# Performance work log

Measured on AMD Instinct MI355X. Metric: run time of the kernel, lower is better.

## Reference

```python
import jax, jax.numpy as jnp
import numpy as np

PATCH_SIZE = 16
PATCH_STRIDE = 8
LEVEL = 3

# pywt db4 decomposition filters (dec_lo, dec_hi)
_DB4_DEC_LO = np.array([-0.010597401784997278, 0.032883011666982945,
                        0.030841381835986965, -0.18703481171888114,
                        -0.02798376941698385, 0.6308807679295904,
                        0.7148465705525415, 0.23037781330885523], dtype=np.float32)
_DB4_DEC_HI = np.array([-0.23037781330885523, 0.7148465705525415,
                        -0.6308807679295904, -0.02798376941698385,
                        0.18703481171888114, 0.030841381835986965,
                        -0.032883011666982945, -0.010597401784997278], dtype=np.float32)


def _swt(x, level):
    """Undecimated (a-trous) SWT with periodic boundary, ptwt convention.
    x: (BN, T) with T divisible by 2**level. Returns [cA_L, cD_L, ..., cD_1]."""
    # torch conv1d is cross-correlation -> use flipped filters (true convolution)
    filt = jnp.stack([jnp.asarray(_DB4_DEC_LO[::-1].copy()),
                      jnp.asarray(_DB4_DEC_HI[::-1].copy())], axis=0)[:, None, :]  # (2,1,8)
    filt = filt.astype(x.dtype)
    flen = filt.shape[-1]
    res_lo = x[:, None, :]  # (BN, 1, T)
    details = []
    for lvl in range(level):
        d = 2 ** lvl
        padl, padr = d * (flen // 2 - 1), d * (flen // 2)
        xp = jnp.concatenate([res_lo[..., -padl:], res_lo, res_lo[..., :padr]], axis=-1)
        res = jax.lax.conv_general_dilated(
            xp, filt, window_strides=(1,), padding='VALID',
            rhs_dilation=(d,), dimension_numbers=('NCH', 'OIH', 'NCH'))  # (BN,2,T)
        res_lo = res[:, :1, :]
        details.append(res[:, 1, :])
    return [res_lo[:, 0, :]] + details[::-1]


def setup_inputs() -> dict:
    key = jax.random.key(0)
    x = jax.random.normal(key, (64, 4096, 32), dtype=jnp.float32)
    return {"x": x}


def reference(x):
    B, T, N = x.shape
    xt = jnp.transpose(x, (0, 2, 1))  # (B, N, T)
    pow2 = 2 ** LEVEL
    pad_len = (-T) % pow2
    if pad_len:
        xt = jnp.pad(xt, ((0, 0), (0, 0), (0, pad_len)), mode='edge')  # replicate
    T_pad = T + pad_len
    coeffs = _swt(xt.reshape(B * N, T_pad), LEVEL)           # (level+1) x (BN, T_pad)
    cs = jnp.stack(coeffs, axis=1).reshape(B, N, LEVEL + 1, T_pad)
    if pad_len:
        cs = cs[..., :T]
    P = (T - PATCH_SIZE) // PATCH_STRIDE + 1
    idx = jnp.arange(P)[:, None] * PATCH_STRIDE + jnp.arange(PATCH_SIZE)[None, :]
    patches = cs[..., idx]                                   # (B, N, L+1, P, p)
    patches = jnp.transpose(patches, (0, 3, 1, 2, 4))        # (B, P, N, L+1, p)
    return patches.reshape(B * P, N * (LEVEL + 1), PATCH_SIZE)
```

## Files before the change

kernel.cpp:

```cpp
#include <hip/hip_runtime.h>


#define T_LEN    4096
#define T_MASK   4095
#define NPATCH   511
#define NCHAN    32
#define NTHREADS 256

__device__ __constant__ float c_lo[8] = {
    -0.010597401784997278f, 0.032883011666982945f, 0.030841381835986965f,
    -0.18703481171888114f, -0.02798376941698385f, 0.6308807679295904f,
    0.7148465705525415f,   0.23037781330885523f};
__device__ __constant__ float c_hi[8] = {
    -0.23037781330885523f, 0.7148465705525415f, -0.6308807679295904f,
    -0.02798376941698385f, 0.18703481171888114f, 0.030841381835986965f,
    -0.032883011666982945f, -0.010597401784997278f};

__device__ __forceinline__ void store_pair(float* __restrict__ out_bn, int cbase,
                                           const float* __restrict__ bufLo,
                                           const float* __restrict__ bufHi, int tid) {
#pragma unroll
    for (int it = 0; it < 16; ++it) {
        const int e4 = tid + it * NTHREADS;
        if (e4 < NPATCH * 8) {
            const int p    = e4 >> 3;
            const int r    = e4 & 7;
            const int csub = r >> 2;
            const int j0   = (r & 3) * 4;
            const float* src = csub ? bufHi : bufLo;
            const float4 v = *(const float4*)&src[8 * p + j0];
            *(float4*)&out_bn[(size_t)p * 2048 + (cbase + csub) * 16 + j0] = v;
        }
    }
}

__global__ __launch_bounds__(NTHREADS, 2) void swt_patch(const float* __restrict__ x,
                                                         float* __restrict__ out) {
    __shared__ float bufX[T_LEN];
    __shared__ float bufA[T_LEN];
    __shared__ float bufDa[T_LEN];
    __shared__ float bufDb[T_LEN];

    const int i = blockIdx.x;
    const int r = i & 7;
    const int q = i >> 3;
    const int b = r + 8 * (q >> 5);
    const int n = q & 31;
    const int tid = threadIdx.x;

    const float* xp = x + (size_t)b * T_LEN * NCHAN + n;
#pragma unroll
    for (int k = 0; k < 16; ++k) {
        const int t = tid + k * NTHREADS;
        bufX[t] = xp[(size_t)t * NCHAN];
    }
    __syncthreads();

    float* out_bn = out + (size_t)b * NPATCH * 2048 + (size_t)n * 64;
    const float4* X4 = (const float4*)bufX;
    const float4* A4 = (const float4*)bufA;

#pragma unroll
    for (int k = 0; k < 4; ++k) {
        const int t4 = 4 * (tid + k * NTHREADS);
        float w[12];
        *(float4*)&w[0] = X4[((t4 - 4) & T_MASK) >> 2];
        *(float4*)&w[4] = X4[t4 >> 2];
        *(float4*)&w[8] = X4[((t4 + 4) & T_MASK) >> 2];
        float4 va, vd;
        float* pa = (float*)&va; float* pd = (float*)&vd;
#pragma unroll
        for (int ii = 0; ii < 4; ++ii) {
            float sa = 0.f, sd = 0.f;
#pragma unroll
            for (int j = 0; j < 8; ++j) {
                const float v = w[ii + 8 - j];
                sa = fmaf(c_lo[j], v, sa);
                sd = fmaf(c_hi[j], v, sd);
            }
            pa[ii] = sa; pd[ii] = sd;
        }
        ((float4*)bufA)[t4 >> 2]  = va;
        ((float4*)bufDa)[t4 >> 2] = vd;
    }
    __syncthreads();

#pragma unroll
    for (int k = 0; k < 4; ++k) {
        const int t4 = 4 * (tid + k * NTHREADS);
        float w[20];
        *(float4*)&w[0]  = A4[((t4 - 8) & T_MASK) >> 2];
        *(float4*)&w[4]  = A4[((t4 - 4) & T_MASK) >> 2];
        *(float4*)&w[8]  = A4[t4 >> 2];
        *(float4*)&w[12] = A4[((t4 + 4) & T_MASK) >> 2];
        *(float4*)&w[16] = A4[((t4 + 8) & T_MASK) >> 2];
        float4 va, vd;
        float* pa = (float*)&va; float* pd = (float*)&vd;
#pragma unroll
        for (int ii = 0; ii < 4; ++ii) {
            float sa = 0.f, sd = 0.f;
#pragma unroll
            for (int j = 0; j < 8; ++j) {
                const float v = w[ii + 16 - 2 * j];
                sa = fmaf(c_lo[j], v, sa);
                sd = fmaf(c_hi[j], v, sd);
            }
            pa[ii] = sa; pd[ii] = sd;
        }
        ((float4*)bufX)[t4 >> 2]  = va;
        ((float4*)bufDb)[t4 >> 2] = vd;
    }
    __syncthreads();

    store_pair(out_bn, 2, bufDb, bufDa, tid);
    __syncthreads();

#pragma unroll
    for (int k = 0; k < 4; ++k) {
        const int t4 = 4 * (tid + k * NTHREADS);
        float w[32];
#pragma unroll
        for (int c4 = 0; c4 < 8; ++c4)
            *(float4*)&w[4 * c4] = X4[((t4 - 12 + 4 * c4) & T_MASK) >> 2];
        float4 va, vd;
        float* pa = (float*)&va; float* pd = (float*)&vd;
#pragma unroll
        for (int ii = 0; ii < 4; ++ii) {
            float sa = 0.f, sd = 0.f;
#pragma unroll
            for (int j = 0; j < 8; ++j) {
                const float v = w[ii + 28 - 4 * j];
                sa = fmaf(c_lo[j], v, sa);
                sd = fmaf(c_hi[j], v, sd);
            }
            pa[ii] = sa; pd[ii] = sd;
        }
        ((float4*)bufA)[t4 >> 2]  = va;
        ((float4*)bufDa)[t4 >> 2] = vd;
    }
    __syncthreads();

    store_pair(out_bn, 0, bufA, bufDa, tid);
}

extern "C" void kernel_launch(void* const* d_in, const int* in_sizes, int n_in,
                              void* d_out, int out_size, void* d_ws, size_t ws_size,
                              hipStream_t stream) {
    const float* x = (const float*)d_in[0];
    float* out = (float*)d_out;
    hipLaunchKernelGGL(swt_patch, dim3(64 * 32), dim3(NTHREADS), 0, stream, x, out);
}
```

Baseline: 318.3 us.

## Tile SWT over time chunks with halo, covering all channels per block

Each block now handles one 64-sample time chunk for all 32 channels of a batch, loading a haloed window with coalesced float4 reads and transposing it into padded shared memory. The three SWT levels are computed on shrinking halo ranges. Results are staged so each block writes a contiguous span of output patches with fully coalesced float4 stores. This replaces the old strided per-channel loads and scattered 64-byte output writes, at the cost of recomputing halo samples and using more, smaller blocks.

```diff
diff --git a/kernel.cpp b/kernel.cpp
--- a/kernel.cpp
+++ b/kernel.cpp
@@ -1,11 +1,19 @@
 #include <hip/hip_runtime.h>
 
 
-#define T_LEN    4096
+#define NTHREADS 256
 #define T_MASK   4095
-#define NPATCH   511
-#define NCHAN    32
-#define NTHREADS 256
+
+#define S_IN  132
+#define S_A1  116
+#define S_A2  108
+#define S_ST  76
+#define OFF_IN 0
+#define OFF_A1 4224
+#define OFF_A2 0
+#define OFF_ST 7936
+#define ST_C   2436
+#define LDS_FLOATS (OFF_ST + 4*ST_C)
 
 __device__ __constant__ float c_lo[8] = {
     -0.010597401784997278f, 0.032883011666982945f, 0.030841381835986965f,
@@ -16,57 +24,42 @@
     -0.02798376941698385f, 0.18703481171888114f, 0.030841381835986965f,
     -0.032883011666982945f, -0.010597401784997278f};
 
-__device__ __forceinline__ void store_pair(float* __restrict__ out_bn, int cbase,
-                                           const float* __restrict__ bufLo,
-                                           const float* __restrict__ bufHi, int tid) {
-#pragma unroll
-    for (int it = 0; it < 16; ++it) {
-        const int e4 = tid + it * NTHREADS;
-        if (e4 < NPATCH * 8) {
-            const int p    = e4 >> 3;
-            const int r    = e4 & 7;
-            const int csub = r >> 2;
-            const int j0   = (r & 3) * 4;
-            const float* src = csub ? bufHi : bufLo;
-            const float4 v = *(const float4*)&src[8 * p + j0];
-            *(float4*)&out_bn[(size_t)p * 2048 + (cbase + csub) * 16 + j0] = v;
-        }
-    }
-}
-
 __global__ __launch_bounds__(NTHREADS, 2) void swt_patch(const float* __restrict__ x,
                                                          float* __restrict__ out) {
-    __shared__ float bufX[T_LEN];
-    __shared__ float bufA[T_LEN];
-    __shared__ float bufDa[T_LEN];
-    __shared__ float bufDb[T_LEN];
+    __shared__ float lds[LDS_FLOATS];
 
-    const int i = blockIdx.x;
-    const int r = i & 7;
-    const int q = i >> 3;
-    const int b = r + 8 * (q >> 5);
-    const int n = q & 31;
+    const int blk = blockIdx.x;
+    const int b   = blk >> 6;
+    const int cid = blk & 63;
+    const int T0  = cid << 6;
+    const int p0  = cid << 3;
     const int tid = threadIdx.x;
 
-    const float* xp = x + (size_t)b * T_LEN * NCHAN + n;
+    const float* xb = x + (size_t)b * (4096 * 32);
+    {
 #pragma unroll
-    for (int k = 0; k < 16; ++k) {
-        const int t = tid + k * NTHREADS;
-        bufX[t] = xp[(size_t)t * NCHAN];
+        for (int it = 0; it < 4; ++it) {
+            const int id = tid + it * NTHREADS;
+            const int i  = id >> 3;
+            const int n0 = (id & 7) * 4;
+            const int t  = (T0 - 23 + i) & T_MASK;
+            const float4 v = *(const float4*)&xb[(size_t)t * 32 + n0];
+            lds[OFF_IN + (n0 + 0) * S_IN + i] = v.x;
+            lds[OFF_IN + (n0 + 1) * S_IN + i] = v.y;
+            lds[OFF_IN + (n0 + 2) * S_IN + i] = v.z;
+            lds[OFF_IN + (n0 + 3) * S_IN + i] = v.w;
+        }
     }
     __syncthreads();
 
-    float* out_bn = out + (size_t)b * NPATCH * 2048 + (size_t)n * 64;
-    const float4* X4 = (const float4*)bufX;
-    const float4* A4 = (const float4*)bufA;
-
-#pragma unroll
-    for (int k = 0; k < 4; ++k) {
-        const int t4 = 4 * (tid + k * NTHREADS);
+    for (int tsk = tid; tsk < 29 * 32; tsk += NTHREADS) {
+        const int n = tsk & 31, q = tsk >> 5;
+        const int trel0 = -20 + 4 * q;
         float w[12];
-        *(float4*)&w[0] = X4[((t4 - 4) & T_MASK) >> 2];
-        *(float4*)&w[4] = X4[t4 >> 2];
-        *(float4*)&w[8] = X4[((t4 + 4) & T_MASK) >> 2];
+        const int base = OFF_IN + n * S_IN + 4 * q;
+        *(float4*)&w[0] = *(const float4*)&lds[base];
+        *(float4*)&w[4] = *(const float4*)&lds[base + 4];
+        *(float4*)&w[8] = *(const float4*)&lds[base + 8];
         float4 va, vd;
         float* pa = (float*)&va; float* pd = (float*)&vd;
 #pragma unroll
@@ -74,26 +67,26 @@
             float sa = 0.f, sd = 0.f;
 #pragma unroll
             for (int j = 0; j < 8; ++j) {
-                const float v = w[ii + 8 - j];
+                const float v = w[ii + 7 - j];
                 sa = fmaf(c_lo[j], v, sa);
                 sd = fmaf(c_hi[j], v, sd);
             }
             pa[ii] = sa; pd[ii] = sd;
         }
-        ((float4*)bufA)[t4 >> 2]  = va;
-        ((float4*)bufDa)[t4 >> 2] = vd;
+        *(float4*)&lds[OFF_A1 + n * S_A1 + (trel0 + 20)] = va;
+        if (trel0 >= 0 && trel0 <= 68)
+            *(float4*)&lds[OFF_ST + 3 * ST_C + n * S_ST + trel0] = vd;
     }
     __syncthreads();
 
+    for (int tsk = tid; tsk < 25 * 32; tsk += NTHREADS) {
+        const int n = tsk & 31, q = tsk >> 5;
+        const int trel0 = -12 + 4 * q;
+        float w[20];
+        const int base = OFF_A1 + n * S_A1 + 4 * q;
 #pragma unroll
-    for (int k = 0; k < 4; ++k) {
-        const int t4 = 4 * (tid + k * NTHREADS);
-        float w[20];
-        *(float4*)&w[0]  = A4[((t4 - 8) & T_MASK) >> 2];
-        *(float4*)&w[4]  = A4[((t4 - 4) & T_MASK) >> 2];
-        *(float4*)&w[8]  = A4[t4 >> 2];
-        *(float4*)&w[12] = A4[((t4 + 4) & T_MASK) >> 2];
-        *(float4*)&w[16] = A4[((t4 + 8) & T_MASK) >> 2];
+        for (int c4 = 0; c4 < 5; ++c4)
+            *(float4*)&w[4 * c4] = *(const float4*)&lds[base + 4 * c4];
         float4 va, vd;
         float* pa = (float*)&va; float* pd = (float*)&vd;
 #pragma unroll
@@ -107,21 +100,20 @@
             }
             pa[ii] = sa; pd[ii] = sd;
         }
-        ((float4*)bufX)[t4 >> 2]  = va;
-        ((float4*)bufDb)[t4 >> 2] = vd;
+        *(float4*)&lds[OFF_A2 + n * S_A2 + (trel0 + 12)] = va;
+        if (trel0 >= 0 && trel0 <= 68)
+            *(float4*)&lds[OFF_ST + 2 * ST_C + n * S_ST + trel0] = vd;
     }
     __syncthreads();
 
-    store_pair(out_bn, 2, bufDb, bufDa, tid);
-    __syncthreads();
-
-#pragma unroll
-    for (int k = 0; k < 4; ++k) {
-        const int t4 = 4 * (tid + k * NTHREADS);
+    for (int tsk = tid; tsk < 18 * 32; tsk += NTHREADS) {
+        const int n = tsk & 31, q = tsk >> 5;
+        const int trel0 = 4 * q;
         float w[32];
+        const int base = OFF_A2 + n * S_A2 + trel0;
 #pragma unroll
         for (int c4 = 0; c4 < 8; ++c4)
-            *(float4*)&w[4 * c4] = X4[((t4 - 12 + 4 * c4) & T_MASK) >> 2];
+            *(float4*)&w[4 * c4] = *(const float4*)&lds[base + 4 * c4];
         float4 va, vd;
         float* pa = (float*)&va; float* pd = (float*)&vd;
 #pragma unroll
@@ -135,12 +127,23 @@
             }
             pa[ii] = sa; pd[ii] = sd;
         }
-        ((float4*)bufA)[t4 >> 2]  = va;
-        ((float4*)bufDa)[t4 >> 2] = vd;
+        *(float4*)&lds[OFF_ST + 0 * ST_C + n * S_ST + trel0] = va;
+        *(float4*)&lds[OFF_ST + 1 * ST_C + n * S_ST + trel0] = vd;
     }
     __syncthreads();
 
-    store_pair(out_bn, 0, bufA, bufDa, tid);
+    float4* out4 = (float4*)(out + ((size_t)b * 511 + p0) * 2048);
+#pragma unroll
+    for (int it = 0; it < 16; ++it) {
+        const int e4 = tid + it * NTHREADS;
+        const int p_local = e4 >> 9;
+        if (p0 + p_local < 511) {
+            const int n  = (e4 >> 4) & 31;
+            const int c  = (e4 >> 2) & 3;
+            const int trel = 8 * p_local + 4 * (e4 & 3);
+            out4[e4] = *(const float4*)&lds[OFF_ST + c * ST_C + n * S_ST + trel];
+        }
+    }
 }
 
 extern "C" void kernel_launch(void* const* d_in, const int* in_sizes, int n_in,
@@ -148,5 +151,5 @@
                               hipStream_t stream) {
     const float* x = (const float*)d_in[0];
     float* out = (float*)d_out;
-    hipLaunchKernelGGL(swt_patch, dim3(64 * 32), dim3(NTHREADS), 0, stream, x, out);
+    hipLaunchKernelGGL(swt_patch, dim3(64 * 64), dim3(NTHREADS), 0, stream, x, out);
 }
```

New measurement: 290.4 us. 1.1x faster.
